# Kernel optimization log

Hardware: AMD Instinct MI355X
Metric: run time of the kernel (lower is better)

The kernel has to match this reference:

```python
import jax, jax.numpy as jnp
import numpy as np

N = 4096      # n_nodes
IN = 256      # in_features
H = 4         # n_heads
F = 64        # out_features (per head)
SLOPE = 0.2   # leaky relu negative slope


def setup_inputs() -> dict:
    key = jax.random.key(0)
    k0, k1, k2, k3 = jax.random.split(key, 4)
    h = jax.random.normal(k0, (N, IN), dtype=jnp.float32)
    adj = jax.random.randint(k1, (N, N), 0, 2, dtype=jnp.int32)
    # ensure every node has at least one neighbor (self-loop) so softmax is defined
    adj = jnp.maximum(adj, jnp.eye(N, dtype=jnp.int32))
    # linear: in_features -> out_features * n_heads (xavier-ish scale)
    W = jax.random.normal(k2, (H * F, IN), dtype=jnp.float32) * np.float32(1.0 / np.sqrt(IN))
    b = jnp.zeros((H * F,), dtype=jnp.float32)
    # attn: Linear(2*F -> 1), weight row vector of size 2F plus scalar bias
    attn_w = jax.random.normal(k3, (2 * F,), dtype=jnp.float32) * np.float32(1.0 / np.sqrt(2 * F))
    attn_b = jnp.zeros((1,), dtype=jnp.float32)
    return {"h": h, "adj_mat": adj, "W": W, "b": b, "attn_w": attn_w, "attn_b": attn_b}


def reference(h, adj_mat, W, b, attn_w, attn_b):
    n = h.shape[0]
    # node projection: [N, H, F]
    g = (h @ W.T + b).reshape(n, H, F)
    # attn(concat(h_i, h_j)) = <a_src, g_i> + <a_dst, g_j> + bias  (decomposed, same math)
    src = jnp.einsum('nhf,f->nh', g, attn_w[:F])   # [N, H] contribution of node i
    dst = jnp.einsum('nhf,f->nh', g, attn_w[F:])   # [N, H] contribution of node j
    e = src[:, None, :] + dst[None, :, :] + attn_b[0]   # [N, N, H]
    e = jnp.where(e >= 0, e, SLOPE * e)                 # leaky relu
    e = jnp.where(adj_mat[:, :, None] != 0, e, -jnp.inf)  # mask non-edges
    a = jax.nn.softmax(e, axis=1)                       # softmax over neighbors j
    out = jnp.einsum('ijh,jhf->ihf', a, g)              # [N, H, F]
    return out.mean(axis=1)                             # average heads -> [N, F]
```

## Files before the change

### kernel.cpp

```cpp
#include <hip/hip_runtime.h>
#include <stdint.h>

constexpr int NODES = 4096;
constexpr int KIN   = 256;
constexpr int NHEAD = 4;
constexpr int NF    = 64;
constexpr int HFQ   = 256;
#define SLOPE 0.2f
#define L2E 1.44269504088896340736f

typedef __attribute__((ext_vector_type(8))) short short8;
typedef __attribute__((ext_vector_type(4))) float floatx4;

static __device__ __forceinline__ unsigned short f2bf(float f) {
  return __builtin_bit_cast(unsigned short, (__bf16)f);
}

__global__ __launch_bounds__(256) void pack_prep_kernel(
    const int* __restrict__ adj, unsigned* __restrict__ bm,
    const float* __restrict__ hin, const float* __restrict__ Win,
    unsigned short* __restrict__ hB, unsigned short* __restrict__ WB) {
  int tid = threadIdx.x;
  if (blockIdx.x < 2048) {
    int wv = blockIdx.x * 4 + (tid >> 6);
    int lane = tid & 63;
    int jw = wv & 127;
    int it = wv >> 7;
    int i = it * 64 + lane;
    const int4* p = reinterpret_cast<const int4*>(adj + (size_t)i * NODES + jw * 32);
    unsigned m = 0;
#pragma unroll
    for (int q = 0; q < 8; ++q) {
      int4 a = p[q];
      m |= (a.x != 0 ? 1u : 0u) << (q * 4);
      m |= (a.y != 0 ? 1u : 0u) << (q * 4 + 1);
      m |= (a.z != 0 ? 1u : 0u) << (q * 4 + 2);
      m |= (a.w != 0 ? 1u : 0u) << (q * 4 + 3);
    }
    bm[(size_t)jw * NODES + i] = m;
  } else {
    int idx = (blockIdx.x - 2048) * 256 + tid;
    const int NH4 = (NODES * KIN) / 4;
    const int NW4 = (HFQ * KIN) / 4;
    if (idx < NH4) {
      float4 v = reinterpret_cast<const float4*>(hin)[idx];
      ushort4 o = { f2bf(v.x), f2bf(v.y), f2bf(v.z), f2bf(v.w) };
      reinterpret_cast<ushort4*>(hB)[idx] = o;
    } else if (idx < NH4 + NW4) {
      int j = idx - NH4;
      float4 v = reinterpret_cast<const float4*>(Win)[j];
      ushort4 o = { f2bf(v.x), f2bf(v.y), f2bf(v.z), f2bf(v.w) };
      reinterpret_cast<ushort4*>(WB)[j] = o;
    }
  }
}

__global__ __launch_bounds__(256) void proj_kernel(
    const unsigned short* __restrict__ hB, const unsigned short* __restrict__ WB,
    const float* __restrict__ bias,
    float* __restrict__ g32, unsigned short* __restrict__ gT3) {
  int wave = threadIdx.x >> 6, lane = threadIdx.x & 63;
  int tile = blockIdx.x * 4 + wave;
  int mt = tile >> 4, nt = tile & 15;
  int m0 = mt * 16, n0 = nt * 16;
  int r = lane & 15, kg = lane >> 4;
  floatx4 acc = {0.f, 0.f, 0.f, 0.f};
  const short8* Ap = reinterpret_cast<const short8*>(hB + (m0 + r) * KIN + kg * 8);
  const short8* Bp = reinterpret_cast<const short8*>(WB + (n0 + r) * KIN + kg * 8);
#pragma unroll
  for (int kb = 0; kb < 8; ++kb) {
    short8 a = Ap[kb * 4];
    short8 b = Bp[kb * 4];
    acc = __builtin_amdgcn_mfma_f32_16x16x32_bf16(a, b, acc, 0, 0, 0);
  }
  int col = n0 + r;
  float bv = bias[col];
  int head = col >> 6, ct = (col & 63) >> 4, c15 = col & 15;
#pragma unroll
  for (int q = 0; q < 4; ++q) {
    int row = m0 + kg * 4 + q;
    float v = acc[q] + bv;
    g32[row * HFQ + col] = v;
    int si = (row >> 5) * 8192 + head * 2048 + ct * 512 +
             (((row >> 3) & 3) * 16 + c15) * 8 + (row & 7);
    gT3[si] = f2bf(v);
  }
}

__global__ __launch_bounds__(256) void srcdst_kernel(
    const float* __restrict__ g32, const float* __restrict__ attn_w,
    const float* __restrict__ attn_b,
    float4* __restrict__ srcP, unsigned* __restrict__ eP) {
  int wave = threadIdx.x >> 6, lane = threadIdx.x & 63;
  int n = blockIdx.x * 4 + wave;
  float aws = attn_w[lane], awd = attn_w[64 + lane];
  float ab = attn_b[0];
#pragma unroll
  for (int hh = 0; hh < NHEAD; ++hh) {
    float v = g32[n * HFQ + hh * NF + lane];
    float s = v * aws, d = v * awd;
#pragma unroll
    for (int m = 32; m >= 1; m >>= 1) {
      s += __shfl_xor(s, m, 64);
      d += __shfl_xor(d, m, 64);
    }
    if (lane == 0) {
      s += ab;
      float4 sp;
      sp.x = exp2f(s * L2E);
      sp.y = exp2f(0.2f * s * L2E);
      sp.z = exp2f(-s * L2E);
      sp.w = 0.f;
      srcP[n * NHEAD + hh] = sp;
      float e1 = exp2f(d * L2E), e2 = exp2f(0.2f * d * L2E);
      eP[hh * NODES + n] = ((unsigned)f2bf(e2) << 16) | (unsigned)f2bf(e1);
    }
  }
}

__global__ __launch_bounds__(256, 8) void attn_kernel(
    const unsigned* __restrict__ bm, const unsigned short* __restrict__ gT3,
    const float4* __restrict__ srcP, const unsigned* __restrict__ eP,
    float* __restrict__ pnum, float* __restrict__ pden, int JP) {
  int tid = threadIdx.x;
  int hh = tid >> 6, lane = tid & 63;
  int il = lane & 15, kg = lane >> 4;
  int part = blockIdx.x, itile = blockIdx.y;
  int jstart = part * JP;
  int i = itile * 16 + il;

  float4 sp = srcP[i * NHEAD + hh];
  float es1 = sp.x, es2 = sp.y, thr = sp.z;

  floatx4 acc0 = {0.f, 0.f, 0.f, 0.f};
  floatx4 acc1 = acc0, acc2 = acc0, acc3 = acc0, accd = acc0;

  short8 ones;
#pragma unroll
  for (int r = 0; r < 8; ++r) ones[r] = (short)0x3F80;

  const unsigned* epb = eP + hh * NODES;
  const unsigned short* Ab = gT3 + hh * 2048;

  int nsteps = JP / 32;
  for (int stp = 0; stp < nsteps; ++stp) {
    int j0 = jstart + stp * 32;
    int jt = j0 >> 5;
    unsigned mwd = bm[(size_t)jt * NODES + i];
    unsigned mb = (mwd >> (kg * 8)) & 0xFFu;
    const unsigned* ep = epb + j0 + kg * 8;
    uint4 ea = *reinterpret_cast<const uint4*>(ep);
    uint4 eb = *reinterpret_cast<const uint4*>(ep + 4);
    unsigned ev[8] = {ea.x, ea.y, ea.z, ea.w, eb.x, eb.y, eb.z, eb.w};
    short8 bfr;
#pragma unroll
    for (int r = 0; r < 8; ++r) {
      float e1f = __builtin_bit_cast(float, ev[r] << 16);
      float e2f = __builtin_bit_cast(float, ev[r] & 0xFFFF0000u);
      bool sel = e1f >= thr;
      float w = (sel ? es1 : es2) * (sel ? e1f : e2f);
      w = (mb & (1u << r)) ? w : 0.f;
      bfr[r] = (short)f2bf(w);
    }
    const unsigned short* At = Ab + (size_t)jt * 8192;
    const short8 a0 = *reinterpret_cast<const short8*>(At + 0 * 512 + lane * 8);
    const short8 a1 = *reinterpret_cast<const short8*>(At + 1 * 512 + lane * 8);
    const short8 a2 = *reinterpret_cast<const short8*>(At + 2 * 512 + lane * 8);
    const short8 a3 = *reinterpret_cast<const short8*>(At + 3 * 512 + lane * 8);
    acc0 = __builtin_amdgcn_mfma_f32_16x16x32_bf16(a0, bfr, acc0, 0, 0, 0);
    acc1 = __builtin_amdgcn_mfma_f32_16x16x32_bf16(a1, bfr, acc1, 0, 0, 0);
    acc2 = __builtin_amdgcn_mfma_f32_16x16x32_bf16(a2, bfr, acc2, 0, 0, 0);
    acc3 = __builtin_amdgcn_mfma_f32_16x16x32_bf16(a3, bfr, acc3, 0, 0, 0);
    accd = __builtin_amdgcn_mfma_f32_16x16x32_bf16(ones, bfr, accd, 0, 0, 0);
  }

  if (kg == 0)
    pden[(size_t)part * (NODES * NHEAD) + i * NHEAD + hh] = accd[0];

  float* pbase = pnum + (size_t)part * (NODES * HFQ) + (size_t)i * HFQ + hh * NF;
#pragma unroll
  for (int q = 0; q < 4; ++q) {
    int c = kg * 4 + q;
    pbase[c] = acc0[q];
    pbase[16 + c] = acc1[q];
    pbase[32 + c] = acc2[q];
    pbase[48 + c] = acc3[q];
  }
}

__global__ __launch_bounds__(256) void combine_kernel(
    const float* __restrict__ pnum, const float* __restrict__ pden,
    float* __restrict__ out, int NP) {
  int idx = blockIdx.x * 256 + threadIdx.x;
  int i = idx >> 6, f = idx & 63;
  float o = 0.f;
#pragma unroll
  for (int hh = 0; hh < NHEAD; ++hh) {
    float num = 0.f, den = 0.f;
    for (int p = 0; p < NP; ++p) {
      num += pnum[p * (NODES * HFQ) + i * HFQ + hh * NF + f];
      den += pden[p * (NODES * NHEAD) + i * NHEAD + hh];
    }
    o += num / den;
  }
  out[idx] = 0.25f * o;
}

extern "C" void kernel_launch(void* const* d_in, const int* in_sizes, int n_in,
                              void* d_out, int out_size, void* d_ws, size_t ws_size,
                              hipStream_t stream) {
  const float* hin = (const float*)d_in[0];
  const int* adj   = (const int*)d_in[1];
  const float* W   = (const float*)d_in[2];
  const float* b   = (const float*)d_in[3];
  const float* aw  = (const float*)d_in[4];
  const float* ab  = (const float*)d_in[5];
  float* out = (float*)d_out;
  char* ws = (char*)d_ws;

  unsigned short* hB  = (unsigned short*)(ws + 0x000000);
  unsigned short* WB  = (unsigned short*)(ws + 0x200000);
  float* g32          = (float*)(ws + 0x400000);
  unsigned short* gT3 = (unsigned short*)(ws + 0x800000);
  float4* srcP        = (float4*)(ws + 0xA00000);
  unsigned* eP        = (unsigned*)(ws + 0xA40000);
  unsigned* bm        = (unsigned*)(ws + 0xA60000);
  float* pden         = (float*)(ws + 0xC60000);
  float* pnum         = (float*)(ws + 0xD00000);
  const size_t base = 0xD00000;

  int NP = 2;
  if (ws_size >= base + 8ull * NODES * HFQ * 4) NP = 8;
  else if (ws_size >= base + 4ull * NODES * HFQ * 4) NP = 4;
  int JP = NODES / NP;

  pack_prep_kernel<<<2048 + 1088, 256, 0, stream>>>(adj, bm, hin, W, hB, WB);
  proj_kernel<<<1024, 256, 0, stream>>>(hB, WB, b, g32, gT3);
  srcdst_kernel<<<1024, 256, 0, stream>>>(g32, aw, ab, srcP, eP);
  attn_kernel<<<dim3(NP, 256), 256, 0, stream>>>(bm, gT3, srcP, eP, pnum, pden, JP);
  combine_kernel<<<1024, 256, 0, stream>>>(pnum, pden, out, NP);
}
```

Before: 80.93 us.

## Fuse src/dst scores into projection, prefetch attention operands, replace branch with fmax

The src/dst attention-score computation is folded into the projection kernel. Each block now computes a 16-row tile for all four heads and reduces the per-head dot products with shuffles, which removes one launch and the fp32 g32 round trip. The attention loop software-prefetches the next step's mask word and exp factors and uses fmaxf of the two leaky-relu branches instead of a threshold compare, which drops the third exponent from srcP. Risks: the projection launches only 256 blocks, so it has less parallelism, and the extra prefetch registers may affect occupancy in the attention kernel.

```diff
diff --git a/kernel.cpp b/kernel.cpp
--- a/kernel.cpp
+++ b/kernel.cpp
@@ -6,7 +6,6 @@
 constexpr int NHEAD = 4;
 constexpr int NF    = 64;
 constexpr int HFQ   = 256;
-#define SLOPE 0.2f
 #define L2E 1.44269504088896340736f
 
 typedef __attribute__((ext_vector_type(8))) short short8;
@@ -57,70 +56,69 @@
 
 __global__ __launch_bounds__(256) void proj_kernel(
     const unsigned short* __restrict__ hB, const unsigned short* __restrict__ WB,
-    const float* __restrict__ bias,
-    float* __restrict__ g32, unsigned short* __restrict__ gT3) {
-  int wave = threadIdx.x >> 6, lane = threadIdx.x & 63;
-  int tile = blockIdx.x * 4 + wave;
-  int mt = tile >> 4, nt = tile & 15;
-  int m0 = mt * 16, n0 = nt * 16;
+    const float* __restrict__ bias, const float* __restrict__ attn_w,
+    const float* __restrict__ attn_b,
+    unsigned short* __restrict__ gT3, float2* __restrict__ srcP,
+    unsigned* __restrict__ eP) {
+  int h = threadIdx.x >> 6, lane = threadIdx.x & 63;
+  int m0 = blockIdx.x * 16;
   int r = lane & 15, kg = lane >> 4;
-  floatx4 acc = {0.f, 0.f, 0.f, 0.f};
+  floatx4 acc[4] = {{0.f,0.f,0.f,0.f},{0.f,0.f,0.f,0.f},{0.f,0.f,0.f,0.f},{0.f,0.f,0.f,0.f}};
   const short8* Ap = reinterpret_cast<const short8*>(hB + (m0 + r) * KIN + kg * 8);
-  const short8* Bp = reinterpret_cast<const short8*>(WB + (n0 + r) * KIN + kg * 8);
 #pragma unroll
   for (int kb = 0; kb < 8; ++kb) {
     short8 a = Ap[kb * 4];
-    short8 b = Bp[kb * 4];
-    acc = __builtin_amdgcn_mfma_f32_16x16x32_bf16(a, b, acc, 0, 0, 0);
-  }
-  int col = n0 + r;
-  float bv = bias[col];
-  int head = col >> 6, ct = (col & 63) >> 4, c15 = col & 15;
-#pragma unroll
-  for (int q = 0; q < 4; ++q) {
-    int row = m0 + kg * 4 + q;
-    float v = acc[q] + bv;
-    g32[row * HFQ + col] = v;
-    int si = (row >> 5) * 8192 + head * 2048 + ct * 512 +
-             (((row >> 3) & 3) * 16 + c15) * 8 + (row & 7);
-    gT3[si] = f2bf(v);
-  }
-}
-
-__global__ __launch_bounds__(256) void srcdst_kernel(
-    const float* __restrict__ g32, const float* __restrict__ attn_w,
-    const float* __restrict__ attn_b,
-    float4* __restrict__ srcP, unsigned* __restrict__ eP) {
-  int wave = threadIdx.x >> 6, lane = threadIdx.x & 63;
-  int n = blockIdx.x * 4 + wave;
-  float aws = attn_w[lane], awd = attn_w[64 + lane];
+#pragma unroll
+    for (int nt = 0; nt < 4; ++nt) {
+      const short8 b = *reinterpret_cast<const short8*>(
+          WB + (h * NF + nt * 16 + r) * KIN + kg * 8 + kb * 32);
+      acc[nt] = __builtin_amdgcn_mfma_f32_16x16x32_bf16(a, b, acc[nt], 0, 0, 0);
+    }
+  }
+  float ps[4] = {0.f,0.f,0.f,0.f}, pd[4] = {0.f,0.f,0.f,0.f};
+#pragma unroll
+  for (int nt = 0; nt < 4; ++nt) {
+    int f = nt * 16 + r;
+    float bv = bias[h * NF + f];
+    float was = attn_w[f], wad = attn_w[64 + f];
+#pragma unroll
+    for (int q = 0; q < 4; ++q) {
+      int row = m0 + kg * 4 + q;
+      float v = acc[nt][q] + bv;
+      int si = (row >> 5) * 8192 + h * 2048 + nt * 512 +
+               (((row >> 3) & 3) * 16 + r) * 8 + (row & 7);
+      gT3[si] = f2bf(v);
+      ps[q] += v * was;
+      pd[q] += v * wad;
+    }
+  }
+#pragma unroll
+  for (int m = 8; m >= 1; m >>= 1) {
+#pragma unroll
+    for (int q = 0; q < 4; ++q) {
+      ps[q] += __shfl_xor(ps[q], m, 64);
+      pd[q] += __shfl_xor(pd[q], m, 64);
+    }
+  }
   float ab = attn_b[0];
-#pragma unroll
-  for (int hh = 0; hh < NHEAD; ++hh) {
-    float v = g32[n * HFQ + hh * NF + lane];
-    float s = v * aws, d = v * awd;
-#pragma unroll
-    for (int m = 32; m >= 1; m >>= 1) {
-      s += __shfl_xor(s, m, 64);
-      d += __shfl_xor(d, m, 64);
-    }
-    if (lane == 0) {
-      s += ab;
-      float4 sp;
+  if ((lane & 15) == 0) {
+#pragma unroll
+    for (int q = 0; q < 4; ++q) {
+      int row = m0 + kg * 4 + q;
+      float s = ps[q] + ab, d = pd[q];
+      float2 sp;
       sp.x = exp2f(s * L2E);
       sp.y = exp2f(0.2f * s * L2E);
-      sp.z = exp2f(-s * L2E);
-      sp.w = 0.f;
-      srcP[n * NHEAD + hh] = sp;
+      srcP[row * NHEAD + h] = sp;
       float e1 = exp2f(d * L2E), e2 = exp2f(0.2f * d * L2E);
-      eP[hh * NODES + n] = ((unsigned)f2bf(e2) << 16) | (unsigned)f2bf(e1);
+      eP[h * NODES + row] = ((unsigned)f2bf(e2) << 16) | (unsigned)f2bf(e1);
     }
   }
 }
 
 __global__ __launch_bounds__(256, 8) void attn_kernel(
     const unsigned* __restrict__ bm, const unsigned short* __restrict__ gT3,
-    const float4* __restrict__ srcP, const unsigned* __restrict__ eP,
+    const float2* __restrict__ srcP, const unsigned* __restrict__ eP,
     float* __restrict__ pnum, float* __restrict__ pden, int JP) {
   int tid = threadIdx.x;
   int hh = tid >> 6, lane = tid & 63;
@@ -129,8 +127,8 @@
   int jstart = part * JP;
   int i = itile * 16 + il;
 
-  float4 sp = srcP[i * NHEAD + hh];
-  float es1 = sp.x, es2 = sp.y, thr = sp.z;
+  float2 sp = srcP[i * NHEAD + hh];
+  float es1 = sp.x, es2 = sp.y;
 
   floatx4 acc0 = {0.f, 0.f, 0.f, 0.f};
   floatx4 acc1 = acc0, acc2 = acc0, acc3 = acc0, accd = acc0;
@@ -139,40 +137,50 @@
 #pragma unroll
   for (int r = 0; r < 8; ++r) ones[r] = (short)0x3F80;
 
-  const unsigned* epb = eP + hh * NODES;
-  const unsigned short* Ab = gT3 + hh * 2048;
+  int jt0 = jstart >> 5;
+  const unsigned* bmp = bm + (size_t)jt0 * NODES + i;
+  const unsigned* epp = eP + hh * NODES + jstart + kg * 8;
+  const unsigned short* Atp = gT3 + (size_t)jt0 * 8192 + hh * 2048 + lane * 8;
+
+  unsigned mwd = *bmp;
+  uint4 ea = *reinterpret_cast<const uint4*>(epp);
+  uint4 eb = *reinterpret_cast<const uint4*>(epp + 4);
 
   int nsteps = JP / 32;
-  for (int stp = 0; stp < nsteps; ++stp) {
-    int j0 = jstart + stp * 32;
-    int jt = j0 >> 5;
-    unsigned mwd = bm[(size_t)jt * NODES + i];
-    unsigned mb = (mwd >> (kg * 8)) & 0xFFu;
-    const unsigned* ep = epb + j0 + kg * 8;
-    uint4 ea = *reinterpret_cast<const uint4*>(ep);
-    uint4 eb = *reinterpret_cast<const uint4*>(ep + 4);
-    unsigned ev[8] = {ea.x, ea.y, ea.z, ea.w, eb.x, eb.y, eb.z, eb.w};
-    short8 bfr;
-#pragma unroll
-    for (int r = 0; r < 8; ++r) {
-      float e1f = __builtin_bit_cast(float, ev[r] << 16);
-      float e2f = __builtin_bit_cast(float, ev[r] & 0xFFFF0000u);
-      bool sel = e1f >= thr;
-      float w = (sel ? es1 : es2) * (sel ? e1f : e2f);
-      w = (mb & (1u << r)) ? w : 0.f;
-      bfr[r] = (short)f2bf(w);
-    }
-    const unsigned short* At = Ab + (size_t)jt * 8192;
-    const short8 a0 = *reinterpret_cast<const short8*>(At + 0 * 512 + lane * 8);
-    const short8 a1 = *reinterpret_cast<const short8*>(At + 1 * 512 + lane * 8);
-    const short8 a2 = *reinterpret_cast<const short8*>(At + 2 * 512 + lane * 8);
-    const short8 a3 = *reinterpret_cast<const short8*>(At + 3 * 512 + lane * 8);
-    acc0 = __builtin_amdgcn_mfma_f32_16x16x32_bf16(a0, bfr, acc0, 0, 0, 0);
-    acc1 = __builtin_amdgcn_mfma_f32_16x16x32_bf16(a1, bfr, acc1, 0, 0, 0);
-    acc2 = __builtin_amdgcn_mfma_f32_16x16x32_bf16(a2, bfr, acc2, 0, 0, 0);
-    acc3 = __builtin_amdgcn_mfma_f32_16x16x32_bf16(a3, bfr, acc3, 0, 0, 0);
-    accd = __builtin_amdgcn_mfma_f32_16x16x32_bf16(ones, bfr, accd, 0, 0, 0);
-  }
+
+#define STEP_BODY {                                                         \
+    unsigned mb = (mwd >> (kg * 8)) & 0xFFu;                                \
+    unsigned ev[8] = {ea.x, ea.y, ea.z, ea.w, eb.x, eb.y, eb.z, eb.w};      \
+    short8 bfr;                                                             \
+    _Pragma("unroll")                                                       \
+    for (int r = 0; r < 8; ++r) {                                           \
+      float e1f = __builtin_bit_cast(float, ev[r] << 16);                   \
+      float e2f = __builtin_bit_cast(float, ev[r] & 0xFFFF0000u);           \
+      float w = fmaxf(es1 * e1f, es2 * e2f);                                \
+      w = (mb & (1u << r)) ? w : 0.f;                                       \
+      bfr[r] = (short)f2bf(w);                                              \
+    }                                                                       \
+    const short8 a0 = *reinterpret_cast<const short8*>(Atp);                \
+    const short8 a1 = *reinterpret_cast<const short8*>(Atp + 512);          \
+    const short8 a2 = *reinterpret_cast<const short8*>(Atp + 1024);         \
+    const short8 a3 = *reinterpret_cast<const short8*>(Atp + 1536);         \
+    acc0 = __builtin_amdgcn_mfma_f32_16x16x32_bf16(a0, bfr, acc0, 0, 0, 0); \
+    acc1 = __builtin_amdgcn_mfma_f32_16x16x32_bf16(a1, bfr, acc1, 0, 0, 0); \
+    acc2 = __builtin_amdgcn_mfma_f32_16x16x32_bf16(a2, bfr, acc2, 0, 0, 0); \
+    acc3 = __builtin_amdgcn_mfma_f32_16x16x32_bf16(a3, bfr, acc3, 0, 0, 0); \
+    accd = __builtin_amdgcn_mfma_f32_16x16x32_bf16(ones, bfr, accd, 0, 0, 0);\
+  }
+
+  for (int stp = 0; stp < nsteps - 1; ++stp) {
+    unsigned mwd_n = bmp[NODES];
+    uint4 ea_n = *reinterpret_cast<const uint4*>(epp + 32);
+    uint4 eb_n = *reinterpret_cast<const uint4*>(epp + 36);
+    STEP_BODY;
+    mwd = mwd_n; ea = ea_n; eb = eb_n;
+    bmp += NODES; epp += 32; Atp += 8192;
+  }
+  STEP_BODY;
+#undef STEP_BODY
 
   if (kg == 0)
     pden[(size_t)part * (NODES * NHEAD) + i * NHEAD + hh] = accd[0];
@@ -220,14 +228,13 @@
 
   unsigned short* hB  = (unsigned short*)(ws + 0x000000);
   unsigned short* WB  = (unsigned short*)(ws + 0x200000);
-  float* g32          = (float*)(ws + 0x400000);
-  unsigned short* gT3 = (unsigned short*)(ws + 0x800000);
-  float4* srcP        = (float4*)(ws + 0xA00000);
-  unsigned* eP        = (unsigned*)(ws + 0xA40000);
-  unsigned* bm        = (unsigned*)(ws + 0xA60000);
-  float* pden         = (float*)(ws + 0xC60000);
-  float* pnum         = (float*)(ws + 0xD00000);
-  const size_t base = 0xD00000;
+  unsigned short* gT3 = (unsigned short*)(ws + 0x400000);
+  float2* srcP        = (float2*)(ws + 0x600000);
+  unsigned* eP        = (unsigned*)(ws + 0x620000);
+  unsigned* bm        = (unsigned*)(ws + 0x640000);
+  float* pden         = (float*)(ws + 0x840000);
+  float* pnum         = (float*)(ws + 0x900000);
+  const size_t base = 0x900000;
 
   int NP = 2;
   if (ws_size >= base + 8ull * NODES * HFQ * 4) NP = 8;
@@ -235,8 +242,7 @@
   int JP = NODES / NP;
 
   pack_prep_kernel<<<2048 + 1088, 256, 0, stream>>>(adj, bm, hin, W, hB, WB);
-  proj_kernel<<<1024, 256, 0, stream>>>(hB, WB, b, g32, gT3);
-  srcdst_kernel<<<1024, 256, 0, stream>>>(g32, aw, ab, srcP, eP);
+  proj_kernel<<<256, 256, 0, stream>>>(hB, WB, b, aw, ab, gT3, srcP, eP);
   attn_kernel<<<dim3(NP, 256), 256, 0, stream>>>(bm, gT3, srcP, eP, pnum, pden, JP);
   combine_kernel<<<1024, 256, 0, stream>>>(pnum, pden, out, NP);
 }
```

After: 71.20 us. -12.0%, faster.
